# Performance work log

Measured on AMD Instinct MI355X. Metric: run time of the kernel, lower is better.

## Reference

```python
import jax, jax.numpy as jnp
import numpy as np

WIRE_DIM = 32
NUM_WIRES = 64
BATCH = 8192


def setup_inputs() -> dict:
    key = jax.random.key(0)
    k1, k2, k3, k4 = jax.random.split(key, 4)
    outputs = jax.random.normal(k1, (BATCH, NUM_WIRES * WIRE_DIM), dtype=jnp.float32)
    tests = jax.random.randint(k2, (BATCH, 2), 0, NUM_WIRES, dtype=jnp.int64)
    W1 = jax.random.normal(k3, (2 * WIRE_DIM, 10), dtype=jnp.float32) * 0.1
    b1 = jnp.zeros((10,), dtype=jnp.float32)
    W2 = jax.random.normal(k4, (10, 1), dtype=jnp.float32) * 0.1
    b2 = jnp.zeros((1,), dtype=jnp.float32)
    return {"outputs": outputs, "tests": tests, "W1": W1, "b1": b1, "W2": W2, "b2": b2}


def reference(outputs, tests, W1, b1, W2, b2):
    B = outputs.shape[0]
    W = outputs.shape[1] // WIRE_DIM          # num_wires
    wires = outputs.reshape(B, W, WIRE_DIM)   # [B, W, D]
    person = tests[:, 0]
    location = tests[:, 1]
    # gather_nd equivalent: person wire vector per batch element
    person_vec = wires[jnp.arange(B), person]                 # [B, D]
    # per-wire concat [person_vec, wire_vec] -> shared tiny MLP, vectorized over wires
    x = jnp.concatenate(
        [jnp.broadcast_to(person_vec[:, None, :], (B, W, WIRE_DIM)), wires], axis=-1
    )                                                          # [B, W, 2D]
    h = jax.nn.relu(jnp.einsum("bwd,dh->bwh", x, W1) + b1)     # [B, W, 10]
    logits = (jnp.einsum("bwh,ho->bwo", h, W2) + b2)[..., 0]   # [B, W]
    # sparse softmax cross entropy with location labels
    loss = -jnp.take_along_axis(jax.nn.log_softmax(logits, axis=-1),
                                location[:, None], axis=-1)[:, 0]  # [B]
    return loss
```

## Files before the change

kernel.cpp:

```cpp
#include <hip/hip_runtime.h>

#define WIRE_DIM  32
#define NUM_WIRES 64
#define BATCH     8192
#define HID       10

__device__ __forceinline__ float rl(float x, int slane) {
    return __uint_as_float(__builtin_amdgcn_readlane(__float_as_uint(x), slane));
}

__global__ __launch_bounds__(256) void isnet_kernel(
    const float* __restrict__ outputs,
    const int*   __restrict__ tests,
    const float* __restrict__ W1,
    const float* __restrict__ b1,
    const float* __restrict__ W2,
    const float* __restrict__ b2,
    float*       __restrict__ out)
{
    __shared__ __align__(16) float sW1t[HID * 64];
    __shared__ float sB1[HID], sW2[HID], sB2;

    const int tid  = threadIdx.x;
    const int lane = tid & 63;
    const int wave = tid >> 6;

    for (int i = tid; i < 64 * HID; i += 256) {
        int d = i / HID, h = i - d * HID;
        sW1t[h * 64 + d] = W1[i];
    }
    if (tid < HID) { sB1[tid] = b1[tid]; sW2[tid] = W2[tid]; }
    if (tid == 0)  sB2 = b2[0];
    __syncthreads();

    const int b = blockIdx.x * 4 + wave;

    const int sp = __builtin_amdgcn_readfirstlane(tests[2 * b]);
    const int sl = __builtin_amdgcn_readfirstlane(tests[2 * b + 1]);

    const float* row = outputs + (size_t)b * (NUM_WIRES * WIRE_DIM) + lane * WIRE_DIM;
    float4 w[8];
    #pragma unroll
    for (int j = 0; j < 8; ++j) w[j] = *(const float4*)(row + 4 * j);

    float acc[HID];
    #pragma unroll
    for (int h = 0; h < HID; ++h) acc[h] = sB1[h];

    #pragma unroll
    for (int j = 0; j < 8; ++j) {
        const float px = rl(w[j].x, sp);
        const float py = rl(w[j].y, sp);
        const float pz = rl(w[j].z, sp);
        const float pw = rl(w[j].w, sp);
        #pragma unroll
        for (int h = 0; h < HID; ++h) {
            float4 wa = *(const float4*)&sW1t[h * 64 + 4 * j];
            float4 wb = *(const float4*)&sW1t[h * 64 + 32 + 4 * j];
            acc[h] += px * wa.x + py * wa.y + pz * wa.z + pw * wa.w
                    + w[j].x * wb.x + w[j].y * wb.y
                    + w[j].z * wb.z + w[j].w * wb.w;
        }
    }

    float v = sB2;
    #pragma unroll
    for (int h = 0; h < HID; ++h) v += fmaxf(acc[h], 0.f) * sW2[h];

    float m = v;
    #pragma unroll
    for (int off = 32; off > 0; off >>= 1) m = fmaxf(m, __shfl_xor(m, off));
    float e = __expf(v - m);
    float s = e;
    #pragma unroll
    for (int off = 32; off > 0; off >>= 1) s += __shfl_xor(s, off);
    float lv = rl(v, sl);
    if (lane == 0) out[b] = m + __logf(s) - lv;
}

extern "C" void kernel_launch(void* const* d_in, const int* in_sizes, int n_in,
                              void* d_out, int out_size, void* d_ws, size_t ws_size,
                              hipStream_t stream) {
    const float* outputs = (const float*)d_in[0];
    const int*   tests   = (const int*)d_in[1];
    const float* W1      = (const float*)d_in[2];
    const float* b1      = (const float*)d_in[3];
    const float* W2      = (const float*)d_in[4];
    const float* b2      = (const float*)d_in[5];
    float* out = (float*)d_out;

    isnet_kernel<<<BATCH / 4, 256, 0, stream>>>(
        outputs, tests, W1, b1, W2, b2, out);
}
```

Measured before the change: 110.0 us.

## Process two batch rows per wave with software-pipelined chunk loads

Each wave now handles two batch elements, so every LDS weight load feeds two accumulator sets. The fully unrolled register preload of the row is replaced by a rolled loop that prefetches the next float4 chunk while computing the current one. The aim is to cut LDS traffic per element and the register pressure from holding the whole row, at the cost of half as many blocks and a loop that loads the first chunk again on its last iteration. The tests array is read as int32, as in the prior code.

```diff
diff --git a/kernel.cpp b/kernel.cpp
--- a/kernel.cpp
+++ b/kernel.cpp
@@ -4,6 +4,7 @@
 #define NUM_WIRES 64
 #define BATCH     8192
 #define HID       10
+#define NB        2
 
 __device__ __forceinline__ float rl(float x, int slane) {
     return __uint_as_float(__builtin_amdgcn_readlane(__float_as_uint(x), slane));
@@ -33,49 +34,73 @@
     if (tid == 0)  sB2 = b2[0];
     __syncthreads();
 
-    const int b = blockIdx.x * 4 + wave;
+    const int b0 = blockIdx.x * (4 * NB) + wave * NB;
 
-    const int sp = __builtin_amdgcn_readfirstlane(tests[2 * b]);
-    const int sl = __builtin_amdgcn_readfirstlane(tests[2 * b + 1]);
+    const int sp0 = __builtin_amdgcn_readfirstlane(tests[2 * b0]);
+    const int sl0 = __builtin_amdgcn_readfirstlane(tests[2 * b0 + 1]);
+    const int sp1 = __builtin_amdgcn_readfirstlane(tests[2 * b0 + 2]);
+    const int sl1 = __builtin_amdgcn_readfirstlane(tests[2 * b0 + 3]);
 
-    const float* row = outputs + (size_t)b * (NUM_WIRES * WIRE_DIM) + lane * WIRE_DIM;
-    float4 w[8];
+    const float* row0 = outputs + (size_t)(b0 + 0) * (NUM_WIRES * WIRE_DIM) + lane * WIRE_DIM;
+    const float* row1 = outputs + (size_t)(b0 + 1) * (NUM_WIRES * WIRE_DIM) + lane * WIRE_DIM;
+
+    float acc0[HID], acc1[HID];
     #pragma unroll
-    for (int j = 0; j < 8; ++j) w[j] = *(const float4*)(row + 4 * j);
+    for (int h = 0; h < HID; ++h) { acc0[h] = sB1[h]; acc1[h] = sB1[h]; }
 
-    float acc[HID];
-    #pragma unroll
-    for (int h = 0; h < HID; ++h) acc[h] = sB1[h];
+    float4 c0 = *(const float4*)(row0);
+    float4 c1 = *(const float4*)(row1);
 
-    #pragma unroll
+    #pragma unroll 1
     for (int j = 0; j < 8; ++j) {
-        const float px = rl(w[j].x, sp);
-        const float py = rl(w[j].y, sp);
-        const float pz = rl(w[j].z, sp);
-        const float pw = rl(w[j].w, sp);
+        const int jn = (j + 1) & 7;
+        float4 n0 = *(const float4*)(row0 + 4 * jn);
+        float4 n1 = *(const float4*)(row1 + 4 * jn);
+
+        const float p0x = rl(c0.x, sp0), p0y = rl(c0.y, sp0),
+                    p0z = rl(c0.z, sp0), p0w = rl(c0.w, sp0);
+        const float p1x = rl(c1.x, sp1), p1y = rl(c1.y, sp1),
+                    p1z = rl(c1.z, sp1), p1w = rl(c1.w, sp1);
+
+        const float* wrow = &sW1t[4 * j];
         #pragma unroll
         for (int h = 0; h < HID; ++h) {
-            float4 wa = *(const float4*)&sW1t[h * 64 + 4 * j];
-            float4 wb = *(const float4*)&sW1t[h * 64 + 32 + 4 * j];
-            acc[h] += px * wa.x + py * wa.y + pz * wa.z + pw * wa.w
-                    + w[j].x * wb.x + w[j].y * wb.y
-                    + w[j].z * wb.z + w[j].w * wb.w;
+            float4 wa = *(const float4*)(wrow + h * 64);
+            float4 wb = *(const float4*)(wrow + h * 64 + 32);
+            acc0[h] += p0x * wa.x + p0y * wa.y + p0z * wa.z + p0w * wa.w
+                     + c0.x * wb.x + c0.y * wb.y + c0.z * wb.z + c0.w * wb.w;
+            acc1[h] += p1x * wa.x + p1y * wa.y + p1z * wa.z + p1w * wa.w
+                     + c1.x * wb.x + c1.y * wb.y + c1.z * wb.z + c1.w * wb.w;
         }
+        c0 = n0; c1 = n1;
     }
 
-    float v = sB2;
-    #pragma unroll
-    for (int h = 0; h < HID; ++h) v += fmaxf(acc[h], 0.f) * sW2[h];
-
-    float m = v;
-    #pragma unroll
-    for (int off = 32; off > 0; off >>= 1) m = fmaxf(m, __shfl_xor(m, off));
-    float e = __expf(v - m);
-    float s = e;
-    #pragma unroll
-    for (int off = 32; off > 0; off >>= 1) s += __shfl_xor(s, off);
-    float lv = rl(v, sl);
-    if (lane == 0) out[b] = m + __logf(s) - lv;
+    {
+        float v = sB2;
+        #pragma unroll
+        for (int h = 0; h < HID; ++h) v += fmaxf(acc0[h], 0.f) * sW2[h];
+        float m = v;
+        #pragma unroll
+        for (int off = 32; off > 0; off >>= 1) m = fmaxf(m, __shfl_xor(m, off));
+        float s = __expf(v - m);
+        #pragma unroll
+        for (int off = 32; off > 0; off >>= 1) s += __shfl_xor(s, off);
+        float lv = rl(v, sl0);
+        if (lane == 0) out[b0] = m + __logf(s) - lv;
+    }
+    {
+        float v = sB2;
+        #pragma unroll
+        for (int h = 0; h < HID; ++h) v += fmaxf(acc1[h], 0.f) * sW2[h];
+        float m = v;
+        #pragma unroll
+        for (int off = 32; off > 0; off >>= 1) m = fmaxf(m, __shfl_xor(m, off));
+        float s = __expf(v - m);
+        #pragma unroll
+        for (int off = 32; off > 0; off >>= 1) s += __shfl_xor(s, off);
+        float lv = rl(v, sl1);
+        if (lane == 0) out[b0 + 1] = m + __logf(s) - lv;
+    }
 }
 
 extern "C" void kernel_launch(void* const* d_in, const int* in_sizes, int n_in,
@@ -89,6 +114,6 @@
     const float* b2      = (const float*)d_in[5];
     float* out = (float*)d_out;
 
-    isnet_kernel<<<BATCH / 4, 256, 0, stream>>>(
+    isnet_kernel<<<BATCH / (4 * NB), 256, 0, stream>>>(
         outputs, tests, W1, b1, W2, b2, out);
 }
```

New measurement: 159.2 us. 44.7% more time.

## Stage wire rows through padded LDS with coalesced loads, read W1 via scalar loads

Applied to the files above, without the earlier changes.

Global loads of each batch row become fully coalesced float4 reads by the whole wave, written into a per-wave LDS buffer padded to a stride of 36 to avoid bank conflicts. Lanes then read their own wire and the person wire from LDS, replacing readlane broadcasts. The shared W1/b1/W2 staging and the block barrier are removed, and weights are read straight from global memory as wave-uniform values. The cost is an extra LDS round trip and 36 KB of LDS per block, which may limit occupancy, and a loop that is no longer unrolled.

```diff
diff --git a/kernel.cpp b/kernel.cpp
--- a/kernel.cpp
+++ b/kernel.cpp
@@ -4,6 +4,7 @@
 #define NUM_WIRES 64
 #define BATCH     8192
 #define HID       10
+#define STRIDE    36
 
 __device__ __forceinline__ float rl(float x, int slane) {
     return __uint_as_float(__builtin_amdgcn_readlane(__float_as_uint(x), slane));
@@ -18,60 +19,56 @@
     const float* __restrict__ b2,
     float*       __restrict__ out)
 {
-    __shared__ __align__(16) float sW1t[HID * 64];
-    __shared__ float sB1[HID], sW2[HID], sB2;
+    __shared__ __align__(16) float stage[4][NUM_WIRES * STRIDE];
 
     const int tid  = threadIdx.x;
     const int lane = tid & 63;
     const int wave = tid >> 6;
-
-    for (int i = tid; i < 64 * HID; i += 256) {
-        int d = i / HID, h = i - d * HID;
-        sW1t[h * 64 + d] = W1[i];
-    }
-    if (tid < HID) { sB1[tid] = b1[tid]; sW2[tid] = W2[tid]; }
-    if (tid == 0)  sB2 = b2[0];
-    __syncthreads();
+    float* buf = stage[wave];
 
     const int b = blockIdx.x * 4 + wave;
 
     const int sp = __builtin_amdgcn_readfirstlane(tests[2 * b]);
     const int sl = __builtin_amdgcn_readfirstlane(tests[2 * b + 1]);
 
-    const float* row = outputs + (size_t)b * (NUM_WIRES * WIRE_DIM) + lane * WIRE_DIM;
-    float4 w[8];
-    #pragma unroll
-    for (int j = 0; j < 8; ++j) w[j] = *(const float4*)(row + 4 * j);
+    const float* grow = outputs + (size_t)b * (NUM_WIRES * WIRE_DIM);
+    {
+        const int r = lane >> 3;
+        const int c = lane & 7;
+        #pragma unroll
+        for (int t = 0; t < 8; ++t) {
+            float4 v = *(const float4*)(grow + t * 256 + lane * 4);
+            *(float4*)&buf[(t * 8 + r) * STRIDE + c * 4] = v;
+        }
+    }
 
     float acc[HID];
     #pragma unroll
-    for (int h = 0; h < HID; ++h) acc[h] = sB1[h];
+    for (int h = 0; h < HID; ++h) acc[h] = b1[h];
 
-    #pragma unroll
+    #pragma unroll 1
     for (int j = 0; j < 8; ++j) {
-        const float px = rl(w[j].x, sp);
-        const float py = rl(w[j].y, sp);
-        const float pz = rl(w[j].z, sp);
-        const float pw = rl(w[j].w, sp);
+        float4 x = *(const float4*)&buf[lane * STRIDE + j * 4];
+        float4 p = *(const float4*)&buf[sp   * STRIDE + j * 4];
+        const float* wp = W1 + (4 * j) * HID;
+        const float* ww = W1 + (32 + 4 * j) * HID;
         #pragma unroll
         for (int h = 0; h < HID; ++h) {
-            float4 wa = *(const float4*)&sW1t[h * 64 + 4 * j];
-            float4 wb = *(const float4*)&sW1t[h * 64 + 32 + 4 * j];
-            acc[h] += px * wa.x + py * wa.y + pz * wa.z + pw * wa.w
-                    + w[j].x * wb.x + w[j].y * wb.y
-                    + w[j].z * wb.z + w[j].w * wb.w;
+            acc[h] += p.x * wp[0 * HID + h] + p.y * wp[1 * HID + h]
+                    + p.z * wp[2 * HID + h] + p.w * wp[3 * HID + h]
+                    + x.x * ww[0 * HID + h] + x.y * ww[1 * HID + h]
+                    + x.z * ww[2 * HID + h] + x.w * ww[3 * HID + h];
         }
     }
 
-    float v = sB2;
+    float v = b2[0];
     #pragma unroll
-    for (int h = 0; h < HID; ++h) v += fmaxf(acc[h], 0.f) * sW2[h];
+    for (int h = 0; h < HID; ++h) v += fmaxf(acc[h], 0.f) * W2[h];
 
     float m = v;
     #pragma unroll
     for (int off = 32; off > 0; off >>= 1) m = fmaxf(m, __shfl_xor(m, off));
-    float e = __expf(v - m);
-    float s = e;
+    float s = __expf(v - m);
     #pragma unroll
     for (int off = 32; off > 0; off >>= 1) s += __shfl_xor(s, off);
     float lv = rl(v, sl);
```

Measured after the change: 103.3 us. -6.1%, faster.
